# Kernel tuning notes

Measured on AMD Instinct MI355X. Metric: run time of the kernel, lower is better.

Reference implementation:

```python
import jax, jax.numpy as jnp
import numpy as np

K = 3          # conv kernel size
PW = 4         # parallel window (pw_height == pw_width)
OC = 128       # out_channels
IC = 128       # in_channels
RANK = 256
STRIDE = PW - K + 1  # 2


def _sdk_weight_map(kernel):
    # kernel: [O, C, K, K] numpy. Concat all (top,left) zero-pad placements into PWxPW.
    O, C, k, _ = kernel.shape
    d = PW - k
    maps = []
    for top in range(d + 1):
        for left in range(d + 1):
            pk = np.zeros((O, C, PW, PW), dtype=kernel.dtype)
            pk[:, :, top:top + k, left:left + k] = kernel
            maps.append(pk.reshape(O, -1))
    return np.concatenate(maps, axis=0)  # [(d+1)^2 * O, C*PW*PW]


def setup_inputs() -> dict:
    rng = np.random.default_rng(0)
    kernel = (rng.standard_normal((OC, IC, K, K)) * 0.05).astype(np.float32)
    W = _sdk_weight_map(kernel)  # [512, 2048]
    u, s, vh = np.linalg.svd(W, full_matrices=False)
    Q = (u[:, :RANK] * s[:RANK]).astype(np.float32)   # u_t @ diag(s_t)
    R = vh[:RANK].astype(np.float32)
    key = jax.random.key(0)
    x = jax.random.normal(key, (32, 128, 64, 64), dtype=jnp.float32)
    return {"x": x, "Q": jnp.asarray(Q), "R": jnp.asarray(R)}


def _slice_and_forward(x, Q, R):
    N, C, H, Wd = x.shape
    s = STRIDE
    pad_v = (H + 2 - PW) % s
    pad_h = (Wd + 2 - PW) % s
    ov = -(-(H + 2 - PW) // s) + 1   # ceil div + 1 (matches math.ceil(...)+1)
    oh = -(-(Wd + 2 - PW) // s) + 1
    xp = jnp.pad(x, ((0, 0), (0, 0), (1, 1 + pad_v), (1, 1 + pad_h)))
    # im2col / unfold: feature layout C slowest, then (i, j) within window -> matches F.unfold
    wins = [xp[:, :, i:i + s * (ov - 1) + 1:s, j:j + s * (oh - 1) + 1:s]
            for i in range(PW) for j in range(PW)]
    patches = jnp.stack(wins, axis=2)                      # [N, C, PW*PW, ov, oh]
    flat = patches.reshape(N, C * PW * PW, ov * oh).transpose(0, 2, 1)  # [N, L, C*PW*PW]
    # F.linear(flat, Q @ R) == (flat @ R^T) @ Q^T  (apply low-rank factors sequentially)
    lin = jnp.einsum('nlr,mr->nlm', jnp.einsum('nlf,rf->nlr', flat, R), Q)  # [N, L, s*s*OC]
    lin = lin.reshape(N, ov, oh, s, s, OC).transpose(0, 1, 3, 2, 4, 5)
    lin = lin.reshape(N, H + pad_v // 2, Wd + pad_h // 2, OC)
    lin = lin.transpose(0, 3, 1, 2)                        # NHWC -> NCHW
    return lin[:, :, :H, :Wd]


def reference(x, Q, R):
    return _slice_and_forward(x, Q, R)
```

## Files before the change

kernel.cpp:

```cpp
#include <hip/hip_runtime.h>
#include <hip/hip_bf16.h>

typedef __attribute__((ext_vector_type(8))) short short8;
typedef __attribute__((ext_vector_type(4))) float f32x4;
typedef unsigned int uint;
typedef __attribute__((ext_vector_type(4))) uint uint4v;

#define AS1 __attribute__((address_space(1)))
#define AS3 __attribute__((address_space(3)))

#define QB_OFF  (1u << 20)
#define XPH_OFF (1310720u)

__device__ __forceinline__ uint bf16r(float f) {
    uint u = __float_as_uint(f);
    u += 0x7FFFu + ((u >> 16) & 1u);
    return u >> 16;
}
__device__ __forceinline__ uint pk2(float lo, float hi) {
    return bf16r(lo) | (bf16r(hi) << 16);
}

__global__ __launch_bounds__(256) void prep_kernel(
    const float* __restrict__ x, const float* __restrict__ Q, const float* __restrict__ R,
    char* __restrict__ Rp4, char* __restrict__ Qp4, char* __restrict__ xph)
{
    const int bid = blockIdx.x, tid = threadIdx.x;
    if (bid < 2048) {
        __shared__ float xt[128 * 65];
        const int n = bid >> 6, h = bid & 63;
        {
            const int c = tid >> 1, half = tid & 1;
            const float4* src = (const float4*)(x + (((size_t)(n * 128 + c) * 64 + h) * 64 + half * 32));
            #pragma unroll
            for (int q = 0; q < 8; ++q) {
                float4 v = src[q];
                float* d = &xt[c * 65 + half * 32 + q * 4];
                d[0] = v.x; d[1] = v.y; d[2] = v.z; d[3] = v.w;
            }
        }
        __syncthreads();
        {
            const int w = tid >> 2, cq = tid & 3;
            uint pw[16];
            #pragma unroll
            for (int m = 0; m < 16; ++m)
                pw[m] = pk2(xt[(cq * 32 + 2 * m) * 65 + w], xt[(cq * 32 + 2 * m + 1) * 65 + w]);
            char* dst = xph + (size_t)n * 1115136 + (size_t)(h + 1) * 16896 + (w + 1) * 256 + cq * 64;
            #pragma unroll
            for (int i = 0; i < 4; ++i) {
                uint4v q4 = { pw[4 * i], pw[4 * i + 1], pw[4 * i + 2], pw[4 * i + 3] };
                *(uint4v*)(dst + i * 16) = q4;
            }
        }
        if (tid < 32) {
            int side = tid >> 4, e = tid & 15;
            uint4v z = {0, 0, 0, 0};
            *(uint4v*)(xph + (size_t)n * 1115136 + (size_t)(h + 1) * 16896 + side * 65 * 256 + e * 16) = z;
        }
        if (h == 0) {
            uint4v z = {0, 0, 0, 0};
            #pragma unroll
            for (int it = 0; it < 9; ++it) {
                int idx = tid + it * 256;
                if (idx < 2112) {
                    int rr = (idx >= 1056) ? 65 : 0;
                    int jj = idx - (rr ? 1056 : 0);
                    int col = jj >> 4, e = jj & 15;
                    *(uint4v*)(xph + (size_t)n * 1115136 + (size_t)rr * 16896 + col * 256 + e * 16) = z;
                }
            }
        }
    } else if (bid < 2304) {
        int g = (bid - 2048) * 256 + tid;
        int hg = g >> 11, p = g & 2047;
        int col = p >> 3;
        int kgx = (p & 7) ^ (col & 7);
        const float* src = R + (size_t)col * 2048 + (((hg & 1) * 64 + kgx * 8) * 16 + (hg >> 1));
        uint pw[4];
        #pragma unroll
        for (int m = 0; m < 4; ++m)
            pw[m] = pk2(src[(2 * m) * 16], src[(2 * m + 1) * 16]);
        uint4v q4 = { pw[0], pw[1], pw[2], pw[3] };
        *(uint4v*)(Rp4 + (size_t)hg * 32768 + p * 16) = q4;
    } else {
        int g = (bid - 2304) * 256 + tid;
        int ks = g >> 11, p = g & 2047;
        int col = p >> 2, unit = p & 3;
        const float4* s = (const float4*)(Q + (size_t)col * 256 + ks * 32 + unit * 8);
        float4 a = s[0], b = s[1];
        uint4v q4 = { pk2(a.x, a.y), pk2(a.z, a.w), pk2(b.x, b.y), pk2(b.z, b.w) };
        *(uint4v*)(Qp4 + (size_t)ks * 32768 + p * 16) = q4;
    }
}

__global__ __launch_bounds__(512, 2) void fused_kernel(
    const char* __restrict__ xph, const char* __restrict__ Rp4,
    const char* __restrict__ Qp4, float* __restrict__ out)
{
    extern __shared__ __align__(16) char lds[];

    const int b0 = blockIdx.x;
    const int b = (b0 & 7) * 32 + (b0 >> 3);
    const int n = b >> 3, vt = b & 7;
    const int tid = threadIdx.x;
    const int wave = tid >> 6, lane = tid & 63;
    const int lr = lane & 15, kg = lane >> 4;
    const int lr7 = lr & 7;
    const int wm = wave >> 2, wn = wave & 3;

    const char* xbase = xph + (size_t)n * 1115136;

    int pdst[4], xoff[4];
    #pragma unroll
    for (int q = 0; q < 4; ++q) {
        int p = q * 512 + tid;
        pdst[q] = p * 16;
        int m = p >> 4, sl = p & 15;
        xoff[q] = (8 * vt + 2 * (m >> 5)) * 16896 + (2 * (m & 31)) * 256 + ((sl ^ (m & 7)) << 4);
    }
    int abase[4], tbase[4];
    #pragma unroll
    for (int mf = 0; mf < 4; ++mf) {
        int m = wm * 64 + mf * 16 + lr;
        abase[mf] = m * 256;
        tbase[mf] = m * 512;
    }
    int bbase[4];
    #pragma unroll
    for (int nf = 0; nf < 4; ++nf) bbase[nf] = (wn * 64 + nf * 16 + lr) * 128;
    int qbase[8];
    #pragma unroll
    for (int nf = 0; nf < 8; ++nf)
        qbase[nf] = ((wn >> 1) * 256 + (nf >> 2) * 128 + (wn & 1) * 64 + (nf & 3) * 16 + lr) * 64;

#define BDMA(hg_, sb_) { _Pragma("unroll") for (int q = 0; q < 4; ++q)                  \
        __builtin_amdgcn_global_load_lds(                                               \
            (const AS1 void*)(Rp4 + (size_t)(hg_) * 32768 + pdst[q]),                   \
            (AS3 void*)(lds + 65536 + (sb_) * 32768 + pdst[q]), 16, 0, 0); }
#define XDMA(g_, sx_) { _Pragma("unroll") for (int q = 0; q < 4; ++q)                   \
        __builtin_amdgcn_global_load_lds(                                               \
            (const AS1 void*)(xbase + xoff[q] + ((g_) >> 2) * 16896 + ((g_) & 3) * 256),\
            (AS3 void*)(lds + (sx_) * 32768 + pdst[q]), 16, 0, 0); }
#define QDMA(ks_, sq_) { _Pragma("unroll") for (int q = 0; q < 4; ++q)                  \
        __builtin_amdgcn_global_load_lds(                                               \
            (const AS1 void*)(Qp4 + (size_t)(ks_) * 32768 + pdst[q]),                   \
            (AS3 void*)(lds + 65536 + (sq_) * 32768 + pdst[q]), 16, 0, 0); }

#define BAR(Nstr) { __builtin_amdgcn_sched_barrier(0);                                  \
        asm volatile("s_waitcnt vmcnt(" Nstr ") lgkmcnt(0)\n\ts_barrier" ::: "memory"); \
        __builtin_amdgcn_sched_barrier(0); }
#define LBAR { __builtin_amdgcn_sched_barrier(0);                                       \
        asm volatile("s_waitcnt lgkmcnt(0)\n\ts_barrier" ::: "memory");                 \
        __builtin_amdgcn_sched_barrier(0); }

    f32x4 acc[4][4];
    #pragma unroll
    for (int i = 0; i < 4; ++i)
        #pragma unroll
        for (int j = 0; j < 4; ++j) acc[i][j] = (f32x4)0.f;

    BDMA(0, 0); XDMA(0, 0); BDMA(1, 1); XDMA(1, 1);
    __builtin_amdgcn_sched_barrier(0);
    asm volatile("s_waitcnt vmcnt(8)\n\ts_barrier" ::: "memory");
    __builtin_amdgcn_sched_barrier(0);

    #pragma unroll
    for (int h = 0; h < 32; ++h) {
        if (h >= 1 && h <= 30) BDMA(h + 1, (h + 1) & 1);
        if ((h & 1) == 0 && h >= 2 && h <= 28) XDMA((h >> 1) + 1, ((h >> 1) + 1) & 1);
        if (h == 31) QDMA(0, 0);
        const char* xs = lds + ((h >> 1) & 1) * 32768;
        const char* bs = lds + 65536 + (h & 1) * 32768;
        #pragma unroll
        for (int u = 0; u < 2; ++u) {
            const int ug = (h & 1) * 2 + u;
            short8 af[4], bf[4];
            #pragma unroll
            for (int mf = 0; mf < 4; ++mf)
                af[mf] = *(const short8*)(xs + abase[mf] + (((ug * 4 + kg) ^ lr7) << 4));
            #pragma unroll
            for (int nf = 0; nf < 4; ++nf)
                bf[nf] = *(const short8*)(bs + bbase[nf] + (((u * 4 + kg) ^ lr7) << 4));
            #pragma unroll
            for (int nf = 0; nf < 4; ++nf)
                #pragma unroll
                for (int mf = 0; mf < 4; ++mf)
                    acc[mf][nf] = __builtin_amdgcn_mfma_f32_16x16x32_bf16(af[mf], bf[nf], acc[mf][nf], 0, 0, 0);
        }
        if ((h & 1) == 0 && h <= 28) { BAR("4") } else { BAR("0") }
    }

    #pragma unroll
    for (int mf = 0; mf < 4; ++mf)
        #pragma unroll
        for (int nf = 0; nf < 4; ++nf)
            #pragma unroll
            for (int r = 0; r < 4; ++r) {
                int row = wm * 64 + mf * 16 + kg * 4 + r;
                int col = wn * 64 + nf * 16 + lr;
                *(ushort*)(lds + row * 512 + ((col * 2) ^ ((row & 7) << 4))) =
                    (ushort)bf16r(acc[mf][nf][r]);
            }
    QDMA(1, 1);
    LBAR

    f32x4 acc2[4][8];
    #pragma unroll
    for (int i = 0; i < 4; ++i)
        #pragma unroll
        for (int j = 0; j < 8; ++j) acc2[i][j] = (f32x4)0.f;
    #pragma unroll
    for (int ks = 0; ks < 8; ++ks) {
        if (ks >= 1 && ks <= 6) QDMA(ks + 1, (ks + 1) & 1);
        const char* qs = lds + 65536 + (ks & 1) * 32768;
        short8 af2[4];
        #pragma unroll
        for (int mf = 0; mf < 4; ++mf)
            af2[mf] = *(const short8*)(lds + tbase[mf] + (((ks * 32 + kg * 8) * 2) ^ (lr7 << 4)));
        #pragma unroll
        for (int nf = 0; nf < 8; ++nf) {
            const short8 bq = *(const short8*)(qs + qbase[nf] + (kg << 4));
            #pragma unroll
            for (int mf = 0; mf < 4; ++mf)
                acc2[mf][nf] = __builtin_amdgcn_mfma_f32_16x16x32_bf16(af2[mf], bq, acc2[mf][nf], 0, 0, 0);
        }
        BAR("0")
    }

    const int si = wn >> 1, ochalf = wn & 1;
    #pragma unroll
    for (int mh = 0; mh < 4; ++mh) {
        LBAR
        if (wm == (mh >> 1)) {
            #pragma unroll
            for (int mfh = 0; mfh < 2; ++mfh) {
                const int mf = (mh & 1) * 2 + mfh;
                #pragma unroll
                for (int q = 0; q < 4; ++q) {
                    const int oc = ochalf * 64 + q * 16 + lr;
                    const int ub = si * 34816 + oc * 272 + (((4 * mfh + kg) ^ (oc & 7)) << 5);
                    f32x4 v0 = { acc2[mf][q][0], acc2[mf][4 + q][0], acc2[mf][q][1], acc2[mf][4 + q][1] };
                    f32x4 v1 = { acc2[mf][q][2], acc2[mf][4 + q][2], acc2[mf][q][3], acc2[mf][4 + q][3] };
                    *(f32x4*)(lds + ub) = v0;
                    *(f32x4*)(lds + ub + 16) = v1;
                }
            }
        }
        LBAR
        #pragma unroll
        for (int it = 0; it < 8; ++it) {
            int uidx = it * 512 + tid;
            int w4 = uidx & 15, oc = (uidx >> 4) & 127, sie = uidx >> 11;
            f32x4 v = *(const f32x4*)(lds + sie * 34816 + oc * 272 + ((w4 ^ (2 * (oc & 7))) << 4));
            *(f32x4*)(out + (size_t)n * 524288 + (size_t)oc * 4096
                          + (8 * vt + 2 * mh + sie) * 64 + w4 * 4) = v;
        }
    }
}

extern "C" void kernel_launch(void* const* d_in, const int* in_sizes, int n_in,
                              void* d_out, int out_size, void* d_ws, size_t ws_size,
                              hipStream_t stream) {
    const float* x = (const float*)d_in[0];
    const float* Q = (const float*)d_in[1];
    const float* R = (const float*)d_in[2];
    float* out = (float*)d_out;

    char* ws = (char*)d_ws;
    char* Rp4 = ws;
    char* Qp4 = ws + QB_OFF;
    char* xph = ws + XPH_OFF;

    prep_kernel<<<2368, 256, 0, stream>>>(x, Q, R, Rp4, Qp4, xph);
    fused_kernel<<<256, 512, 131072, stream>>>(xph, Rp4, Qp4, out);
}
```

Before: 77.64 us.

## Deepen first-GEMM pipeline to 4-stage ring with finer K steps

Reorganizes the first GEMM (patches × R^T) mainloop to use 64 smaller K steps with a 4-slot LDS ring buffer and three loads in flight, instead of 32 steps with double buffering. The R prepacking layout is changed to match smaller 16 KB chunks, and the X DMA becomes a single load per thread. The LDS layout is repacked so Q prefetch starts during the tail of the first GEMM, and a swizzle is added for the intermediate tile. The aim is to hide global-to-LDS latency better, at the cost of more barriers per unit of work.

```diff
diff --git a/kernel.cpp b/kernel.cpp
--- a/kernel.cpp
+++ b/kernel.cpp
@@ -73,16 +73,15 @@
         }
     } else if (bid < 2304) {
         int g = (bid - 2048) * 256 + tid;
-        int hg = g >> 11, p = g & 2047;
-        int col = p >> 3;
-        int kgx = (p & 7) ^ (col & 7);
-        const float* src = R + (size_t)col * 2048 + (((hg & 1) * 64 + kgx * 8) * 16 + (hg >> 1));
+        int s = g >> 10, p = g & 1023;
+        int col = p >> 2, wu = p & 3;
+        const float* src = R + (size_t)col * 2048 + (((s & 3) * 32 + wu * 8) * 16 + (s >> 2));
         uint pw[4];
         #pragma unroll
         for (int m = 0; m < 4; ++m)
             pw[m] = pk2(src[(2 * m) * 16], src[(2 * m + 1) * 16]);
         uint4v q4 = { pw[0], pw[1], pw[2], pw[3] };
-        *(uint4v*)(Rp4 + (size_t)hg * 32768 + p * 16) = q4;
+        *(uint4v*)(Rp4 + (size_t)s * 16384 + p * 16) = q4;
     } else {
         int g = (bid - 2304) * 256 + tid;
         int ks = g >> 11, p = g & 2047;
@@ -100,8 +99,8 @@
 {
     extern __shared__ __align__(16) char lds[];
 
-    const int b0 = blockIdx.x;
-    const int b = (b0 & 7) * 32 + (b0 >> 3);
+    const int blk = blockIdx.x;
+    const int b = (blk & 7) * 32 + (blk >> 3);
     const int n = b >> 3, vt = b & 7;
     const int tid = threadIdx.x;
     const int wave = tid >> 6, lane = tid & 63;
@@ -110,42 +109,34 @@
     const int wm = wave >> 2, wn = wave & 3;
 
     const char* xbase = xph + (size_t)n * 1115136;
-
-    int pdst[4], xoff[4];
-    #pragma unroll
-    for (int q = 0; q < 4; ++q) {
-        int p = q * 512 + tid;
-        pdst[q] = p * 16;
-        int m = p >> 4, sl = p & 15;
-        xoff[q] = (8 * vt + 2 * (m >> 5)) * 16896 + (2 * (m & 31)) * 256 + ((sl ^ (m & 7)) << 4);
-    }
-    int abase[4], tbase[4];
-    #pragma unroll
-    for (int mf = 0; mf < 4; ++mf) {
-        int m = wm * 64 + mf * 16 + lr;
-        abase[mf] = m * 256;
-        tbase[mf] = m * 512;
-    }
-    int bbase[4];
-    #pragma unroll
-    for (int nf = 0; nf < 4; ++nf) bbase[nf] = (wn * 64 + nf * 16 + lr) * 128;
+    const int u16 = tid * 16;
+
+    const int xm = tid >> 2, xcu = tid & 3;
+    const int xc = (8 * vt + 2 * (xm >> 5)) * 16896 + (2 * (xm & 31)) * 256 + xcu * 16;
+
+    const int a0 = wm * 4096 + lr * 64 + kg * 16;
+    const int bb0 = wn * 4096 + lr * 64 + kg * 16;
+
+    int tb[4];
+    #pragma unroll
+    for (int mf = 0; mf < 4; ++mf) tb[mf] = (wm * 64 + mf * 16 + lr) * 512;
+    const int tswz = (lr7 << 4) ^ ((lr & 8) << 2);
     int qbase[8];
     #pragma unroll
     for (int nf = 0; nf < 8; ++nf)
-        qbase[nf] = ((wn >> 1) * 256 + (nf >> 2) * 128 + (wn & 1) * 64 + (nf & 3) * 16 + lr) * 64;
-
-#define BDMA(hg_, sb_) { _Pragma("unroll") for (int q = 0; q < 4; ++q)                  \
+        qbase[nf] = ((wn >> 1) * 256 + (nf >> 2) * 128 + (wn & 1) * 64 + (nf & 3) * 16 + lr) * 64 + kg * 16;
+
+#define BDMA2(s_) { _Pragma("unroll") for (int q = 0; q < 2; ++q)                       \
         __builtin_amdgcn_global_load_lds(                                               \
-            (const AS1 void*)(Rp4 + (size_t)(hg_) * 32768 + pdst[q]),                   \
-            (AS3 void*)(lds + 65536 + (sb_) * 32768 + pdst[q]), 16, 0, 0); }
-#define XDMA(g_, sx_) { _Pragma("unroll") for (int q = 0; q < 4; ++q)                   \
+            (const AS1 void*)(Rp4 + (size_t)(s_) * 16384 + q * 8192 + u16),             \
+            (AS3 void*)(lds + 32768 + ((s_) & 3) * 16384 + q * 8192 + u16), 16, 0, 0); }
+#define XDMA1(s_) __builtin_amdgcn_global_load_lds(                                     \
+        (const AS1 void*)(xbase + xc + ((s_) >> 4) * 16896 + (((s_) >> 2) & 3) * 256 + ((s_) & 3) * 64), \
+        (AS3 void*)(lds + ((s_) & 3) * 8192 + u16), 16, 0, 0);
+#define QDMA(ks_) { _Pragma("unroll") for (int q = 0; q < 4; ++q)                       \
         __builtin_amdgcn_global_load_lds(                                               \
-            (const AS1 void*)(xbase + xoff[q] + ((g_) >> 2) * 16896 + ((g_) & 3) * 256),\
-            (AS3 void*)(lds + (sx_) * 32768 + pdst[q]), 16, 0, 0); }
-#define QDMA(ks_, sq_) { _Pragma("unroll") for (int q = 0; q < 4; ++q)                  \
-        __builtin_amdgcn_global_load_lds(                                               \
-            (const AS1 void*)(Qp4 + (size_t)(ks_) * 32768 + pdst[q]),                   \
-            (AS3 void*)(lds + 65536 + (sq_) * 32768 + pdst[q]), 16, 0, 0); }
+            (const AS1 void*)(Qp4 + (size_t)(ks_) * 32768 + q * 8192 + u16),            \
+            (AS3 void*)(lds + (((ks_) & 1) ? 65536 : 98304) + q * 8192 + u16), 16, 0, 0); }
 
 #define BAR(Nstr) { __builtin_amdgcn_sched_barrier(0);                                  \
         asm volatile("s_waitcnt vmcnt(" Nstr ") lgkmcnt(0)\n\ts_barrier" ::: "memory"); \
@@ -160,37 +151,34 @@
         #pragma unroll
         for (int j = 0; j < 4; ++j) acc[i][j] = (f32x4)0.f;
 
-    BDMA(0, 0); XDMA(0, 0); BDMA(1, 1); XDMA(1, 1);
-    __builtin_amdgcn_sched_barrier(0);
-    asm volatile("s_waitcnt vmcnt(8)\n\ts_barrier" ::: "memory");
-    __builtin_amdgcn_sched_barrier(0);
-
-    #pragma unroll
-    for (int h = 0; h < 32; ++h) {
-        if (h >= 1 && h <= 30) BDMA(h + 1, (h + 1) & 1);
-        if ((h & 1) == 0 && h >= 2 && h <= 28) XDMA((h >> 1) + 1, ((h >> 1) + 1) & 1);
-        if (h == 31) QDMA(0, 0);
-        const char* xs = lds + ((h >> 1) & 1) * 32768;
-        const char* bs = lds + 65536 + (h & 1) * 32768;
-        #pragma unroll
-        for (int u = 0; u < 2; ++u) {
-            const int ug = (h & 1) * 2 + u;
-            short8 af[4], bf[4];
+    BDMA2(0) XDMA1(0) BDMA2(1) XDMA1(1) BDMA2(2) XDMA1(2)
+    BAR("6")
+
+    #pragma unroll
+    for (int s = 0; s < 64; ++s) {
+        if (s <= 60) { BDMA2(s + 3) XDMA1(s + 3) }
+        if (s == 60) QDMA(0)
+        const char* xs = lds + (s & 3) * 8192;
+        const char* bs = lds + 32768 + (s & 3) * 16384;
+        short8 af[4], bf[4];
+        #pragma unroll
+        for (int mf = 0; mf < 4; ++mf)
+            af[mf] = *(const short8*)(xs + a0 + mf * 1024);
+        #pragma unroll
+        for (int nf = 0; nf < 4; ++nf)
+            bf[nf] = *(const short8*)(bs + bb0 + nf * 1024);
+        #pragma unroll
+        for (int nf = 0; nf < 4; ++nf)
             #pragma unroll
             for (int mf = 0; mf < 4; ++mf)
-                af[mf] = *(const short8*)(xs + abase[mf] + (((ug * 4 + kg) ^ lr7) << 4));
-            #pragma unroll
-            for (int nf = 0; nf < 4; ++nf)
-                bf[nf] = *(const short8*)(bs + bbase[nf] + (((u * 4 + kg) ^ lr7) << 4));
-            #pragma unroll
-            for (int nf = 0; nf < 4; ++nf)
-                #pragma unroll
-                for (int mf = 0; mf < 4; ++mf)
-                    acc[mf][nf] = __builtin_amdgcn_mfma_f32_16x16x32_bf16(af[mf], bf[nf], acc[mf][nf], 0, 0, 0);
-        }
-        if ((h & 1) == 0 && h <= 28) { BAR("4") } else { BAR("0") }
-    }
-
+                acc[mf][nf] = __builtin_amdgcn_mfma_f32_16x16x32_bf16(af[mf], bf[nf], acc[mf][nf], 0, 0, 0);
+        if (s <= 59)      { BAR("6") }
+        else if (s == 60) { BAR("10") }
+        else if (s == 61) { BAR("7") }
+        else              { BAR("4") }
+    }
+
+    QDMA(1)
     #pragma unroll
     for (int mf = 0; mf < 4; ++mf)
         #pragma unroll
@@ -199,11 +187,11 @@
             for (int r = 0; r < 4; ++r) {
                 int row = wm * 64 + mf * 16 + kg * 4 + r;
                 int col = wn * 64 + nf * 16 + lr;
-                *(ushort*)(lds + row * 512 + ((col * 2) ^ ((row & 7) << 4))) =
+                *(ushort*)(lds + row * 512 +
+                           ((col * 2) ^ ((row & 7) << 4) ^ ((row & 8) << 2))) =
                     (ushort)bf16r(acc[mf][nf][r]);
             }
-    QDMA(1, 1);
-    LBAR
+    BAR("4")
 
     f32x4 acc2[4][8];
     #pragma unroll
@@ -212,20 +200,20 @@
         for (int j = 0; j < 8; ++j) acc2[i][j] = (f32x4)0.f;
     #pragma unroll
     for (int ks = 0; ks < 8; ++ks) {
-        if (ks >= 1 && ks <= 6) QDMA(ks + 1, (ks + 1) & 1);
-        const char* qs = lds + 65536 + (ks & 1) * 32768;
+        if (ks >= 1 && ks <= 6) QDMA(ks + 1)
+        const char* qs = lds + ((ks & 1) ? 65536 : 98304);
         short8 af2[4];
         #pragma unroll
         for (int mf = 0; mf < 4; ++mf)
-            af2[mf] = *(const short8*)(lds + tbase[mf] + (((ks * 32 + kg * 8) * 2) ^ (lr7 << 4)));
+            af2[mf] = *(const short8*)(lds + tb[mf] + ((ks * 64 + kg * 16) ^ tswz));
         #pragma unroll
         for (int nf = 0; nf < 8; ++nf) {
-            const short8 bq = *(const short8*)(qs + qbase[nf] + (kg << 4));
+            const short8 bq = *(const short8*)(qs + qbase[nf]);
             #pragma unroll
             for (int mf = 0; mf < 4; ++mf)
                 acc2[mf][nf] = __builtin_amdgcn_mfma_f32_16x16x32_bf16(af2[mf], bq, acc2[mf][nf], 0, 0, 0);
         }
-        BAR("0")
+        if (ks <= 6) { BAR("0") }
     }
 
     const int si = wn >> 1, ochalf = wn & 1;
```

New measurement: 80.60 us. +3.8%, slower.
